# Kernel tuning notes

Hardware: AMD Instinct MI355X
Metric: run time of the kernel (lower is better)

The kernel has to match this reference:

```python
import jax, jax.numpy as jnp
import numpy as np

ALPHA = 0.2  # LeakyReLU negative slope
NEG_INF = jnp.float32(-9e15)


def gat_layer(h, mask, W, a, concat):
    """Dense GAT layer (pyGAT style). h: [B,N,Fin], mask: [N,N] bool, W: [Fin,Fout], a: [2*Fout,1]."""
    Wh = h @ W                                   # [B,N,Fout]
    F_out = W.shape[-1]
    e_src = Wh @ a[:F_out]                       # [B,N,1]
    e_dst = Wh @ a[F_out:]                       # [B,N,1]
    e = jax.nn.leaky_relu(e_src + jnp.swapaxes(e_dst, -1, -2), ALPHA)  # [B,N,N]
    att = jnp.where(mask, e, NEG_INF)
    att = jax.nn.softmax(att, axis=-1)
    out = att @ Wh                               # [B,N,Fout]
    return jax.nn.elu(out) if concat else out


def setup_inputs() -> dict:
    key = jax.random.key(0)
    ks = jax.random.split(key, 8)
    B, N, nfeat, nhid, nheads, emb, nclass = 4, 2048, 128, 64, 8, 64, 16
    slices = jax.random.normal(ks[0], (B, N, nfeat), jnp.float32)
    adj = jax.random.randint(ks[1], (N, N), 0, 2, jnp.int32)
    s = 1.0 / float(np.sqrt(nfeat))
    Ws = jax.random.uniform(ks[2], (nheads, nfeat, nhid), jnp.float32, -s, s)
    As = jax.random.uniform(ks[3], (nheads, 2 * nhid, 1), jnp.float32, -s, s)
    W1 = jax.random.uniform(ks[4], (nhid * nheads, emb), jnp.float32, -s, s)
    a1 = jax.random.uniform(ks[5], (2 * emb, 1), jnp.float32, -s, s)
    W2 = jax.random.uniform(ks[6], (emb, nclass), jnp.float32, -s, s)
    a2 = jax.random.uniform(ks[7], (2 * nclass, 1), jnp.float32, -s, s)
    return {"slices": slices, "adj": adj, "Ws": Ws, "As": As,
            "W1": W1, "a1": a1, "W2": W2, "a2": a2}


def reference(slices, adj, Ws, As, W1, a1, W2, a2):
    # Eval mode: dropout = 0 (identity).
    mask = adj > 0                               # [N,N], broadcasts over batch
    # Multi-head GAT with concat=True (ELU inside each head), vectorized over heads.
    heads = jax.vmap(lambda W, a: gat_layer(slices, mask, W, a, True))(Ws, As)  # [H,B,N,nhid]
    H, B, N, nh = heads.shape
    x = jnp.moveaxis(heads, 0, 2).reshape(B, N, H * nh)  # concat along features, head-major
    image_feature = jax.nn.elu(gat_layer(x, mask, W1, a1, False))              # [B,N,emb]
    pre = jax.nn.elu(gat_layer(image_feature, mask, W2, a2, False))            # [B,N,nclass]
    pre = pre[:, 0, :]                                                         # [B,nclass]
    return image_feature, pre
```

## Files before the change

### kernel.cpp

```cpp
#include <hip/hip_runtime.h>
#include <hip/hip_bf16.h>
#include <cstdint>


#define NN 2048

typedef float f32x4 __attribute__((ext_vector_type(4)));
typedef __bf16 bf16x8 __attribute__((ext_vector_type(8)));
typedef _Float16 f16;
typedef _Float16 f16x8 __attribute__((ext_vector_type(8)));

__device__ __forceinline__ unsigned pkbf(float a, float b) {
  __hip_bfloat162 t = __float22bfloat162_rn(make_float2(a, b));
  unsigned r;
  __builtin_memcpy(&r, &t, 4);
  return r;
}

__global__ __launch_bounds__(256) void prep_k(
    const int* __restrict__ adj, unsigned short* __restrict__ plane,
    const float* __restrict__ Ws, __bf16* __restrict__ WsFh, __bf16* __restrict__ WsFl,
    const float* __restrict__ W1, __bf16* __restrict__ W1Fh, __bf16* __restrict__ W1Fl) {
  const int bx = blockIdx.x, t = threadIdx.x;
  if (bx < 2048) {
    const long base = (long)bx * NN;
#pragma unroll
    for (int jt = 0; jt < 8; ++jt) {
      const int j = jt * 256 + t;
      plane[base + j] = adj[base + j] > 0 ? 0xFFFFu : 0u;
    }
  } else if (bx < 2304) {
    const int idx = (bx - 2048) * 256 + t;
    const int inst = idx >> 13;
    const int rem = idx & 8191;
    const int k = rem >> 6, n = rem & 63;
    const float v = Ws[(long)inst * 8192 + rem];
    const __bf16 vh = (__bf16)v;
    const int pos = ((k >> 5) * 4 + (n >> 4)) * 512 + (((k >> 3) & 3) * 16 + (n & 15)) * 8 + (k & 7);
    WsFh[(long)inst * 8192 + pos] = vh;
    WsFl[(long)inst * 8192 + pos] = (__bf16)(v - (float)vh);
  } else {
    const int idx = (bx - 2304) * 256 + t;
    const int k = idx >> 6, n = idx & 63;
    const float v = W1[idx];
    const __bf16 vh = (__bf16)v;
    const int pos = ((k >> 5) * 4 + (n >> 4)) * 512 + (((k >> 3) & 3) * 16 + (n & 15)) * 8 + (k & 7);
    W1Fh[pos] = vh;
    W1Fl[pos] = (__bf16)(v - (float)vh);
  }
}

struct GemmLd {
  float4 a0, a1;
  bf16x8 bh[4], bl[4];
};

__global__ __launch_bounds__(128) void gemm_mfma_k(
    const float* __restrict__ Aall, const __bf16* __restrict__ WFhi,
    const __bf16* __restrict__ WFlo, const float* __restrict__ avecAll,
    f16* __restrict__ WhBAll, float* __restrict__ Eo, float* __restrict__ Go,
    f16* __restrict__ Fo, f16* __restrict__ Ho, float* __restrict__ pC,
    int K, int KS, long aStrideB) {
  const int p = blockIdx.y;
  const int ks = blockIdx.z;
  const float* A = Aall + (long)(p & 3) * aStrideB;
  const long wfOff = (long)(p >> 2) * K * 64;
  const bf16x8* BhF = (const bf16x8*)(WFhi + wfOff);
  const bf16x8* BlF = (const bf16x8*)(WFlo + wfOff);

  const int t = threadIdx.x, lane = t & 63, wave = t >> 6;
  const int quad = lane >> 4, lm = lane & 15;
  const int i0w = blockIdx.x * 32 + wave * 16;
  const float* Arow = A + (long)(i0w + lm) * K;
  const int kBeg = ks * (K / KS), kEnd = kBeg + K / KS;

  f32x4 acc[4];
#pragma unroll
  for (int nt = 0; nt < 4; ++nt) acc[nt] = (f32x4){0.f, 0.f, 0.f, 0.f};

  auto LOAD = [&](GemmLd& L, int k0) {
    L.a0 = *(const float4*)(Arow + k0 + quad * 8);
    L.a1 = *(const float4*)(Arow + k0 + quad * 8 + 4);
    const int bbase = (k0 >> 5) * 256 + lane;
#pragma unroll
    for (int nt = 0; nt < 4; ++nt) {
      L.bh[nt] = BhF[bbase + nt * 64];
      L.bl[nt] = BlF[bbase + nt * 64];
    }
  };
  auto STEP = [&](const GemmLd& L) {
    const float av8[8] = {L.a0.x, L.a0.y, L.a0.z, L.a0.w, L.a1.x, L.a1.y, L.a1.z, L.a1.w};
    bf16x8 ah, al;
#pragma unroll
    for (int j = 0; j < 8; ++j) {
      const __bf16 h = (__bf16)av8[j];
      ah[j] = h;
      al[j] = (__bf16)(av8[j] - (float)h);
    }
#pragma unroll
    for (int nt = 0; nt < 4; ++nt) {
      acc[nt] = __builtin_amdgcn_mfma_f32_16x16x32_bf16(ah, L.bh[nt], acc[nt], 0, 0, 0);
      acc[nt] = __builtin_amdgcn_mfma_f32_16x16x32_bf16(al, L.bh[nt], acc[nt], 0, 0, 0);
      acc[nt] = __builtin_amdgcn_mfma_f32_16x16x32_bf16(ah, L.bl[nt], acc[nt], 0, 0, 0);
    }
  };

  GemmLd La, Lb;
  LOAD(La, kBeg);
  for (int k0 = kBeg; k0 < kEnd; k0 += 64) {
    LOAD(Lb, k0 + 32);
    STEP(La);
    LOAD(La, (k0 + 64 < kEnd) ? k0 + 64 : kBeg);
    STEP(Lb);
  }

  if (KS > 1) {
    float* pc = pC + ((long)(p * KS + ks) * NN) * 64;
#pragma unroll
    for (int reg = 0; reg < 4; ++reg) {
      const int row = i0w + quad * 4 + reg;
#pragma unroll
      for (int nt = 0; nt < 4; ++nt) pc[(long)row * 64 + nt * 16 + lm] = acc[nt][reg];
    }
    return;
  }

  const float* av = avecAll + (long)(p >> 2) * 128;
  f16* WhB = WhBAll + (long)p * NN * 64;
  float* E = Eo + (long)p * NN;
  float* G = Go + (long)p * NN;
  f16* F = Fo + (long)p * NN;
  f16* Hh = Ho + (long)p * NN;

  float alo[4], ahi[4];
#pragma unroll
  for (int nt = 0; nt < 4; ++nt) {
    alo[nt] = av[nt * 16 + lm];
    ahi[nt] = av[64 + nt * 16 + lm];
  }
#pragma unroll
  for (int reg = 0; reg < 4; ++reg) {
    float es = 0.f, ed = 0.f;
#pragma unroll
    for (int nt = 0; nt < 4; ++nt) {
      es += acc[nt][reg] * alo[nt];
      ed += acc[nt][reg] * ahi[nt];
    }
#pragma unroll
    for (int m = 1; m < 16; m <<= 1) {
      es += __shfl_xor(es, m);
      ed += __shfl_xor(ed, m);
    }
    if (lm == 0) {
      const int r = i0w + quad * 4 + reg;
      E[r] = __expf(es);
      G[r] = __expf(0.2f * es);
      F[r] = (f16)__expf(ed);
      Hh[r] = (f16)__expf(0.2f * ed);
    }
  }

  const int r0 = i0w + quad * 4;
  const long base = ((long)(r0 >> 5) * 4) * 512 + (((r0 >> 3) & 3) * 16 + lm) * 8 + (r0 & 7);
#pragma unroll
  for (int nt = 0; nt < 4; ++nt) {
    union { f16 h[4]; uint2 u; } pk;
#pragma unroll
    for (int q = 0; q < 4; ++q) pk.h[q] = (f16)acc[nt][q];
    *(uint2*)(WhB + base + nt * 512) = pk.u;
  }
}

__global__ __launch_bounds__(256) void gemm_epi_k(
    const float* __restrict__ pC, const float* __restrict__ avec,
    f16* __restrict__ WhBAll, float* __restrict__ Eo, float* __restrict__ Go,
    f16* __restrict__ Fo, f16* __restrict__ Ho, int KS) {
  const int inst = blockIdx.y;
  const int t = threadIdx.x;
  const int row = blockIdx.x * 16 + (t >> 4);
  const int cg = t & 15;
  f32x4 c = (f32x4){0.f, 0.f, 0.f, 0.f};
  for (int ks = 0; ks < KS; ++ks)
    c += *(const f32x4*)(pC + (((long)(inst * KS + ks) * NN) + row) * 64 + cg * 4);
  float es = 0.f, ed = 0.f;
#pragma unroll
  for (int q = 0; q < 4; ++q) {
    const int n = cg * 4 + q;
    es += c[q] * avec[n];
    ed += c[q] * avec[64 + n];
  }
#pragma unroll
  for (int m = 1; m < 16; m <<= 1) {
    es += __shfl_xor(es, m);
    ed += __shfl_xor(ed, m);
  }
  if (cg == 0) {
    Eo[(long)inst * NN + row] = __expf(es);
    Go[(long)inst * NN + row] = __expf(0.2f * es);
    Fo[(long)inst * NN + row] = (f16)__expf(ed);
    Ho[(long)inst * NN + row] = (f16)__expf(0.2f * ed);
  }
  f16* WhB = WhBAll + (long)inst * NN * 64;
#pragma unroll
  for (int q = 0; q < 4; ++q) {
    const int n = cg * 4 + q;
    const int pos = ((row >> 5) * 4 + (n >> 4)) * 512 + (((row >> 3) & 3) * 16 + (n & 15)) * 8 + (row & 7);
    WhB[pos] = (f16)c[q];
  }
}

struct AttnLd {
  f16x8 F, H;
  uint4 m0, m1;
  f16x8 b[4];
};

__global__ __launch_bounds__(512) void attn_k(
    const f16* __restrict__ WhBAll, const float* __restrict__ Eb,
    const float* __restrict__ Gb, const f16* __restrict__ Fb,
    const f16* __restrict__ Hb, const unsigned short* __restrict__ plane,
    float* __restrict__ out1, float* __restrict__ out2, int rowStride, long strideB,
    int jsCount, float* __restrict__ partAcc, float* __restrict__ partSum) {
  const int p = blockIdx.z;
  const int js = blockIdx.y;
  const f16x8* bp = (const f16x8*)(WhBAll + (long)p * NN * 64);
  const float* E = Eb + (long)p * NN;
  const float* G = Gb + (long)p * NN;
  const f16* F = Fb + (long)p * NN;
  const f16* Hv = Hb + (long)p * NN;
  const int t = threadIdx.x, lane = t & 63, wave = t >> 6;
  const int rw = wave & 3;
  const int half = wave >> 2;
  const int quad = lane >> 4, lm = lane & 15;
  const int i0 = blockIdx.x * 128 + rw * 32;
  const int span = 64 / jsCount;
  const int kbBeg = js * span + half * (span / 2);
  const int kbEnd = kbBeg + span / 2;

  const f16 e0 = (f16)E[i0 + lm], g0 = (f16)G[i0 + lm];
  const f16 e1 = (f16)E[i0 + 16 + lm], g1 = (f16)G[i0 + 16 + lm];
  f16x8 e0v, g0v, e1v, g1v;
#pragma unroll
  for (int j = 0; j < 8; ++j) { e0v[j] = e0; g0v[j] = g0; e1v[j] = e1; g1v[j] = g1; }
  const unsigned short* mp0 = plane + (long)(i0 + lm) * NN;
  const unsigned short* mp1 = plane + (long)(i0 + 16 + lm) * NN;

  f16x8 ones;
#pragma unroll
  for (int j = 0; j < 8; ++j) ones[j] = (lm == 0) ? (f16)1.0f : (f16)0.0f;

  f32x4 acc0[4], acc1[4], sum0, sum1;
#pragma unroll
  for (int nt = 0; nt < 4; ++nt) {
    acc0[nt] = (f32x4){0.f, 0.f, 0.f, 0.f};
    acc1[nt] = (f32x4){0.f, 0.f, 0.f, 0.f};
  }
  sum0 = (f32x4){0.f, 0.f, 0.f, 0.f};
  sum1 = (f32x4){0.f, 0.f, 0.f, 0.f};

  auto LOAD = [&](AttnLd& L, int kb) {
    const int c0 = kb * 32 + quad * 8;
    L.F = *(const f16x8*)(F + c0);
    L.H = *(const f16x8*)(Hv + c0);
    L.m0 = *(const uint4*)(mp0 + c0);
    L.m1 = *(const uint4*)(mp1 + c0);
#pragma unroll
    for (int nt = 0; nt < 4; ++nt) L.b[nt] = bp[(kb * 4 + nt) * 64 + lane];
  };
  auto STEP = [&](const AttnLd& L) {
    union { f16x8 v; uint4 u; } A0, A1;
    A0.v = __builtin_elementwise_max(e0v * L.F, g0v * L.H);
    A1.v = __builtin_elementwise_max(e1v * L.F, g1v * L.H);
    A0.u.x &= L.m0.x; A0.u.y &= L.m0.y; A0.u.z &= L.m0.z; A0.u.w &= L.m0.w;
    A1.u.x &= L.m1.x; A1.u.y &= L.m1.y; A1.u.z &= L.m1.z; A1.u.w &= L.m1.w;
#pragma unroll
    for (int nt = 0; nt < 4; ++nt) {
      acc0[nt] = __builtin_amdgcn_mfma_f32_16x16x32_f16(A0.v, L.b[nt], acc0[nt], 0, 0, 0);
      acc1[nt] = __builtin_amdgcn_mfma_f32_16x16x32_f16(A1.v, L.b[nt], acc1[nt], 0, 0, 0);
    }
    sum0 = __builtin_amdgcn_mfma_f32_16x16x32_f16(A0.v, ones, sum0, 0, 0, 0);
    sum1 = __builtin_amdgcn_mfma_f32_16x16x32_f16(A1.v, ones, sum1, 0, 0, 0);
  };

  AttnLd La, Lb;
  LOAD(La, kbBeg);
  for (int kb = kbBeg; kb < kbEnd; kb += 2) {
    LOAD(Lb, kb + 1);
    STEP(La);
    LOAD(La, (kb + 2 < kbEnd) ? kb + 2 : kbBeg);
    STEP(Lb);
  }

  __shared__ float cmb[4 * 64 * 40];
  if (half == 1) {
    float* dst = &cmb[(rw * 64 + lane) * 40];
#pragma unroll
    for (int nt = 0; nt < 4; ++nt) {
      *(f32x4*)(dst + nt * 4) = acc0[nt];
      *(f32x4*)(dst + 16 + nt * 4) = acc1[nt];
    }
    *(f32x4*)(dst + 32) = sum0;
    *(f32x4*)(dst + 36) = sum1;
  }
  __syncthreads();
  if (half == 1) return;
  {
    const float* src = &cmb[(rw * 64 + lane) * 40];
#pragma unroll
    for (int nt = 0; nt < 4; ++nt) {
      acc0[nt] += *(const f32x4*)(src + nt * 4);
      acc1[nt] += *(const f32x4*)(src + 16 + nt * 4);
    }
    sum0 += *(const f32x4*)(src + 32);
    sum1 += *(const f32x4*)(src + 36);
  }

  if (jsCount == 1) {
#pragma unroll
    for (int g = 0; g < 2; ++g) {
      const f32x4* acc = g ? acc1 : acc0;
      const f32x4 sm = g ? sum1 : sum0;
#pragma unroll
      for (int reg = 0; reg < 4; ++reg) {
        const int row = i0 + g * 16 + quad * 4 + reg;
        const float ls = __shfl(sm[reg], quad * 16);
        const float il = ls > 0.f ? 1.f / ls : 0.f;
#pragma unroll
        for (int nt = 0; nt < 4; ++nt) {
          float v = acc[nt][reg] * il;
          v = v > 0.f ? v : expm1f(v);
          const long o = (long)(p & 3) * strideB + (long)row * rowStride + (p >> 2) * 64 + nt * 16 + lm;
          out1[o] = v;
          if (out2) out2[o] = v;
        }
      }
    }
  } else {
    float* pAcc = partAcc + ((long)p * jsCount + js) * NN * 64;
    float* pSum = partSum + ((long)p * jsCount + js) * NN;
#pragma unroll
    for (int g = 0; g < 2; ++g) {
      const f32x4* acc = g ? acc1 : acc0;
      const f32x4 sm = g ? sum1 : sum0;
#pragma unroll
      for (int reg = 0; reg < 4; ++reg) {
        const int row = i0 + g * 16 + quad * 4 + reg;
#pragma unroll
        for (int nt = 0; nt < 4; ++nt) pAcc[(long)row * 64 + nt * 16 + lm] = acc[nt][reg];
        if (lm == 0) pSum[row] = sm[reg];
      }
    }
  }
}

__global__ __launch_bounds__(256) void combine_k(const float* __restrict__ partAcc,
                                                 const float* __restrict__ partSum,
                                                 float* __restrict__ img,
                                                 float* __restrict__ out, int JS) {
  const long idx = (long)blockIdx.x * 256 + threadIdx.x;
  const int cg = idx & 15;
  const int row = (int)((idx >> 4) & (NN - 1));
  const int inst = (int)(idx >> 15);
  f32x4 v = (f32x4){0.f, 0.f, 0.f, 0.f};
  float s = 0.f;
  for (int js = 0; js < JS; ++js) {
    const long b = ((long)inst * JS + js) * NN;
    v += *(const f32x4*)(partAcc + (b + row) * 64 + cg * 4);
    s += partSum[b + row];
  }
  const float il = s > 0.f ? 1.f / s : 0.f;
  f32x4 r;
#pragma unroll
  for (int q = 0; q < 4; ++q) {
    float x = v[q] * il;
    r[q] = x > 0.f ? x : expm1f(x);
  }
  const long o = ((long)inst * NN + row) * 64 + cg * 4;
  *(f32x4*)(img + o) = r;
  *(f32x4*)(out + o) = r;
}

__global__ __launch_bounds__(256) void layer3a_k(
    const float* __restrict__ img, const float* __restrict__ W2,
    const float* __restrict__ a2, const unsigned short* __restrict__ plane,
    float* __restrict__ pOut ) {
  const int bb = blockIdx.x, chunk = blockIdx.y, t = threadIdx.x;
  const float* A = img + (long)bb * NN * 64;
  __shared__ float w2alo[64], w2ahi[64];
  __shared__ float W2s[64][17];
  __shared__ float redc[4][17];
  if (t < 64) {
    float sl = 0.f, sh = 0.f;
#pragma unroll
    for (int c = 0; c < 16; ++c) {
      const float wv = W2[t * 16 + c];
      W2s[t][c] = wv;
      sl += wv * a2[c];
      sh += wv * a2[16 + c];
    }
    w2alo[t] = sl;
    w2ahi[t] = sh;
  }
  __syncthreads();

  float es = 0.f;
#pragma unroll 16
  for (int k = 0; k < 64; ++k) es += A[k] * w2alo[k];

  const int j = chunk * 256 + t;
  float arow[64];
#pragma unroll
  for (int q = 0; q < 16; ++q) *(f32x4*)(arow + q * 4) = *(const f32x4*)(A + (long)j * 64 + q * 4);
  float ed = 0.f;
#pragma unroll
  for (int k = 0; k < 64; ++k) ed += arow[k] * w2ahi[k];
  float e = es + ed;
  e = fmaxf(e, 0.2f * e);
  const float pv = plane[j] ? __expf(e) : 0.f;

  float acc[16];
#pragma unroll
  for (int c = 0; c < 16; ++c) {
    float wh = 0.f;
#pragma unroll
    for (int k = 0; k < 64; ++k) wh += arow[k] * W2s[k][c];
    acc[c] = pv * wh;
  }
  float lsum = pv;

#pragma unroll
  for (int off = 32; off > 0; off >>= 1) {
    lsum += __shfl_down(lsum, off);
#pragma unroll
    for (int c = 0; c < 16; ++c) acc[c] += __shfl_down(acc[c], off);
  }
  if ((t & 63) == 0) {
    const int wv = t >> 6;
#pragma unroll
    for (int c = 0; c < 16; ++c) redc[wv][c] = acc[c];
    redc[wv][16] = lsum;
  }
  __syncthreads();
  if (t < 17) {
    pOut[((long)bb * 8 + chunk) * 17 + t] =
        redc[0][t] + redc[1][t] + redc[2][t] + redc[3][t];
  }
}

__global__ __launch_bounds__(64) void layer3b_k(const float* __restrict__ pOut,
                                                float* __restrict__ outPre) {
  const int t = threadIdx.x;
  if (t >= 64) return;
  const int bb = t >> 4, c = t & 15;
  float a = 0.f, l = 0.f;
#pragma unroll
  for (int ch = 0; ch < 8; ++ch) {
    a += pOut[((long)bb * 8 + ch) * 17 + c];
    l += pOut[((long)bb * 8 + ch) * 17 + 16];
  }
  float v = a / l;
  v = v > 0.f ? v : expm1f(v);
  outPre[bb * 16 + c] = v;
}

extern "C" void kernel_launch(void* const* d_in, const int* in_sizes, int n_in,
                              void* d_out, int out_size, void* d_ws, size_t ws_size,
                              hipStream_t stream) {
  (void)in_sizes; (void)n_in; (void)out_size; (void)ws_size;
  constexpr int B = 4, N = NN, JS2 = 4, KS2 = 4;

  const float* slices = (const float*)d_in[0];
  const int* adj = (const int*)d_in[1];
  const float* Ws = (const float*)d_in[2];
  const float* As = (const float*)d_in[3];
  const float* W1 = (const float*)d_in[4];
  const float* a1 = (const float*)d_in[5];
  const float* W2 = (const float*)d_in[6];
  const float* a2 = (const float*)d_in[7];
  float* out = (float*)d_out;

  char* w = (char*)d_ws;
  size_t off = 0;
  auto alloc = [&](size_t bytes) {
    void* ptr = w + off;
    off += (bytes + 255) & ~(size_t)255;
    return ptr;
  };
  unsigned short* plane = (unsigned short*)alloc((size_t)N * N * 2);
  __bf16* WsFh = (__bf16*)alloc((size_t)8 * 128 * 64 * 2);
  __bf16* WsFl = (__bf16*)alloc((size_t)8 * 128 * 64 * 2);
  __bf16* W1Fh = (__bf16*)alloc((size_t)512 * 64 * 2);
  __bf16* W1Fl = (__bf16*)alloc((size_t)512 * 64 * 2);
  f16* WhB1 = (f16*)alloc((size_t)32 * N * 64 * 2);
  float* E1 = (float*)alloc((size_t)32 * N * 4);
  float* G1 = (float*)alloc((size_t)32 * N * 4);
  f16* F1 = (f16*)alloc((size_t)32 * N * 2);
  f16* H1 = (f16*)alloc((size_t)32 * N * 2);
  float* x = (float*)alloc((size_t)B * N * 512 * 4);
  float* pC2 = (float*)alloc((size_t)B * KS2 * N * 64 * 4);
  f16* WhB2 = (f16*)alloc((size_t)B * N * 64 * 2);
  float* E2 = (float*)alloc((size_t)B * N * 4);
  float* G2 = (float*)alloc((size_t)B * N * 4);
  f16* F2 = (f16*)alloc((size_t)B * N * 2);
  f16* H2 = (f16*)alloc((size_t)B * N * 2);
  float* img = (float*)alloc((size_t)B * N * 64 * 4);
  float* pAcc2 = (float*)alloc((size_t)B * JS2 * N * 64 * 4);
  float* pSum2 = (float*)alloc((size_t)B * JS2 * N * 4);
  float* pL3 = (float*)alloc((size_t)B * 8 * 17 * 4);

  prep_k<<<dim3(2432), dim3(256), 0, stream>>>(adj, plane, Ws, WsFh, WsFl, W1, W1Fh, W1Fl);

  gemm_mfma_k<<<dim3(N / 32, 32, 1), dim3(128), 0, stream>>>(
      slices, WsFh, WsFl, As, WhB1, E1, G1, F1, H1, (float*)nullptr,
      128, 1, (long)N * 128);
  attn_k<<<dim3(N / 128, 1, 32), dim3(512), 0, stream>>>(
      WhB1, E1, G1, F1, H1, plane, x, (float*)nullptr, 512, (long)N * 512,
      1, (float*)nullptr, (float*)nullptr);

  gemm_mfma_k<<<dim3(N / 32, 4, KS2), dim3(128), 0, stream>>>(
      x, W1Fh, W1Fl, a1, (f16*)nullptr, (float*)nullptr, (float*)nullptr,
      (f16*)nullptr, (f16*)nullptr, pC2, 512, KS2, (long)N * 512);
  gemm_epi_k<<<dim3(N / 16, 4), dim3(256), 0, stream>>>(
      pC2, a1, WhB2, E2, G2, F2, H2, KS2);
  attn_k<<<dim3(N / 128, JS2, 4), dim3(512), 0, stream>>>(
      WhB2, E2, G2, F2, H2, plane, (float*)nullptr, (float*)nullptr, 64, (long)N * 64,
      JS2, pAcc2, pSum2);
  combine_k<<<dim3(B * N * 16 / 256), dim3(256), 0, stream>>>(pAcc2, pSum2, img, out, JS2);

  layer3a_k<<<dim3(B, 8), dim3(256), 0, stream>>>(img, W2, a2, plane, pL3);
  layer3b_k<<<dim3(1), dim3(64), 0, stream>>>(pL3, out + (size_t)B * N * 64);
}
```

Baseline: 192.0 us.

## Stage attention operands in LDS via global_load_lds with byte-packed tiled mask

New measurement: 165.0 us. 14.0% less time.

```diff
diff --git a/kernel.cpp b/kernel.cpp
--- a/kernel.cpp
+++ b/kernel.cpp
@@ -10,24 +10,24 @@
 typedef _Float16 f16;
 typedef _Float16 f16x8 __attribute__((ext_vector_type(8)));
 
-__device__ __forceinline__ unsigned pkbf(float a, float b) {
-  __hip_bfloat162 t = __float22bfloat162_rn(make_float2(a, b));
-  unsigned r;
-  __builtin_memcpy(&r, &t, 4);
-  return r;
+__device__ __forceinline__ void gll16(const void* g, void* l) {
+  __builtin_amdgcn_global_load_lds(
+      (const __attribute__((address_space(1))) unsigned int*)g,
+      (__attribute__((address_space(3))) unsigned int*)l, 16, 0, 0);
 }
 
 __global__ __launch_bounds__(256) void prep_k(
-    const int* __restrict__ adj, unsigned short* __restrict__ plane,
+    const int* __restrict__ adj, unsigned char* __restrict__ pm,
     const float* __restrict__ Ws, __bf16* __restrict__ WsFh, __bf16* __restrict__ WsFl,
     const float* __restrict__ W1, __bf16* __restrict__ W1Fh, __bf16* __restrict__ W1Fl) {
   const int bx = blockIdx.x, t = threadIdx.x;
   if (bx < 2048) {
-    const long base = (long)bx * NN;
+    const int i = bx;
 #pragma unroll
     for (int jt = 0; jt < 8; ++jt) {
       const int j = jt * 256 + t;
-      plane[base + j] = adj[base + j] > 0 ? 0xFFFFu : 0u;
+      pm[((long)(j >> 5) << 16) + i * 32 + (j & 31)] =
+          adj[(long)i * NN + j] > 0 ? 0xFFu : 0u;
     }
   } else if (bx < 2304) {
     const int idx = (bx - 2048) * 256 + t;
@@ -209,45 +209,59 @@
   }
 }
 
-struct AttnLd {
-  f16x8 F, H;
-  uint4 m0, m1;
-  f16x8 b[4];
-};
-
 __global__ __launch_bounds__(512) void attn_k(
     const f16* __restrict__ WhBAll, const float* __restrict__ Eb,
     const float* __restrict__ Gb, const f16* __restrict__ Fb,
-    const f16* __restrict__ Hb, const unsigned short* __restrict__ plane,
+    const f16* __restrict__ Hb, const unsigned char* __restrict__ pm,
     float* __restrict__ out1, float* __restrict__ out2, int rowStride, long strideB,
     int jsCount, float* __restrict__ partAcc, float* __restrict__ partSum) {
   const int p = blockIdx.z;
   const int js = blockIdx.y;
-  const f16x8* bp = (const f16x8*)(WhBAll + (long)p * NN * 64);
+  const f16* WhB = WhBAll + (long)p * NN * 64;
   const float* E = Eb + (long)p * NN;
   const float* G = Gb + (long)p * NN;
   const f16* F = Fb + (long)p * NN;
   const f16* Hv = Hb + (long)p * NN;
   const int t = threadIdx.x, lane = t & 63, wave = t >> 6;
-  const int rw = wave & 3;
-  const int half = wave >> 2;
+  const int rw = wave & 3, half = wave >> 2;
   const int quad = lane >> 4, lm = lane & 15;
-  const int i0 = blockIdx.x * 128 + rw * 32;
+  const int i0 = blockIdx.x * 128;
+  const int rbase = rw * 32;
   const int span = 64 / jsCount;
-  const int kbBeg = js * span + half * (span / 2);
-  const int kbEnd = kbBeg + span / 2;
-
-  const f16 e0 = (f16)E[i0 + lm], g0 = (f16)G[i0 + lm];
-  const f16 e1 = (f16)E[i0 + 16 + lm], g1 = (f16)G[i0 + 16 + lm];
+  const int nIter = span / 2;
+  const int kbBeg = js * span + half * nIter;
+
+  __shared__ __align__(16) char pool[40960];
+  f16* Fs = (f16*)pool;
+  f16* Hs = (f16*)(pool + 4096);
+  char* ring = pool + 8192 + half * 16384;
+
+  const int r0g = i0 + rbase + lm, r1g = i0 + rbase + 16 + lm;
+  const f16 e0 = (f16)E[r0g], g0 = (f16)G[r0g];
+  const f16 e1 = (f16)E[r1g], g1 = (f16)G[r1g];
   f16x8 e0v, g0v, e1v, g1v;
 #pragma unroll
   for (int j = 0; j < 8; ++j) { e0v[j] = e0; g0v[j] = g0; e1v[j] = e1; g1v[j] = g1; }
-  const unsigned short* mp0 = plane + (long)(i0 + lm) * NN;
-  const unsigned short* mp1 = plane + (long)(i0 + 16 + lm) * NN;
 
   f16x8 ones;
 #pragma unroll
   for (int j = 0; j < 8; ++j) ones[j] = (lm == 0) ? (f16)1.0f : (f16)0.0f;
+
+  if (wave == 0) {
+#pragma unroll
+    for (int q = 0; q < 4; ++q) gll16((const char*)F + q * 1024 + lane * 16, pool + q * 1024);
+#pragma unroll
+    for (int q = 0; q < 4; ++q) gll16((const char*)Hv + q * 1024 + lane * 16, pool + 4096 + q * 1024);
+  }
+  if (rw == 0) {
+    const char* gB = (const char*)WhB + (long)kbBeg * 4096;
+    const unsigned char* gM = pm + ((long)kbBeg << 16) + i0 * 32;
+#pragma unroll
+    for (int q = 0; q < 4; ++q) gll16(gB + q * 1024 + lane * 16, ring + q * 1024);
+#pragma unroll
+    for (int q = 0; q < 4; ++q) gll16(gM + q * 1024 + lane * 16, ring + 4096 + q * 1024);
+  }
+  __syncthreads();
 
   f32x4 acc0[4], acc1[4], sum0, sum1;
 #pragma unroll
@@ -258,40 +272,47 @@
   sum0 = (f32x4){0.f, 0.f, 0.f, 0.f};
   sum1 = (f32x4){0.f, 0.f, 0.f, 0.f};
 
-  auto LOAD = [&](AttnLd& L, int kb) {
-    const int c0 = kb * 32 + quad * 8;
-    L.F = *(const f16x8*)(F + c0);
-    L.H = *(const f16x8*)(Hv + c0);
-    L.m0 = *(const uint4*)(mp0 + c0);
-    L.m1 = *(const uint4*)(mp1 + c0);
-#pragma unroll
-    for (int nt = 0; nt < 4; ++nt) L.b[nt] = bp[(kb * 4 + nt) * 64 + lane];
-  };
-  auto STEP = [&](const AttnLd& L) {
+  for (int i = 0; i < nIter; ++i) {
+    const int kb = kbBeg + i;
+    if (rw == 0 && i + 1 < nIter) {
+      char* dst = ring + ((i + 1) & 1) * 8192;
+      const char* gB = (const char*)WhB + (long)(kb + 1) * 4096;
+      const unsigned char* gM = pm + ((long)(kb + 1) << 16) + i0 * 32;
+#pragma unroll
+      for (int q = 0; q < 4; ++q) gll16(gB + q * 1024 + lane * 16, dst + q * 1024);
+#pragma unroll
+      for (int q = 0; q < 4; ++q) gll16(gM + q * 1024 + lane * 16, dst + 4096 + q * 1024);
+    }
+    const char* slot = ring + (i & 1) * 8192;
+    const f16x8 F8 = *(const f16x8*)(Fs + kb * 32 + quad * 8);
+    const f16x8 H8 = *(const f16x8*)(Hs + kb * 32 + quad * 8);
+    const uint2 m0 = *(const uint2*)(slot + 4096 + (rbase + lm) * 32 + quad * 8);
+    const uint2 m1 = *(const uint2*)(slot + 4096 + (rbase + 16 + lm) * 32 + quad * 8);
+
     union { f16x8 v; uint4 u; } A0, A1;
-    A0.v = __builtin_elementwise_max(e0v * L.F, g0v * L.H);
-    A1.v = __builtin_elementwise_max(e1v * L.F, g1v * L.H);
-    A0.u.x &= L.m0.x; A0.u.y &= L.m0.y; A0.u.z &= L.m0.z; A0.u.w &= L.m0.w;
-    A1.u.x &= L.m1.x; A1.u.y &= L.m1.y; A1.u.z &= L.m1.z; A1.u.w &= L.m1.w;
+    A0.v = __builtin_elementwise_max(e0v * F8, g0v * H8);
+    A1.v = __builtin_elementwise_max(e1v * F8, g1v * H8);
+    A0.u.x &= __builtin_amdgcn_perm(0u, m0.x, 0x01010000u);
+    A0.u.y &= __builtin_amdgcn_perm(0u, m0.x, 0x03030202u);
+    A0.u.z &= __builtin_amdgcn_perm(0u, m0.y, 0x01010000u);
+    A0.u.w &= __builtin_amdgcn_perm(0u, m0.y, 0x03030202u);
+    A1.u.x &= __builtin_amdgcn_perm(0u, m1.x, 0x01010000u);
+    A1.u.y &= __builtin_amdgcn_perm(0u, m1.x, 0x03030202u);
+    A1.u.z &= __builtin_amdgcn_perm(0u, m1.y, 0x01010000u);
+    A1.u.w &= __builtin_amdgcn_perm(0u, m1.y, 0x03030202u);
+
 #pragma unroll
     for (int nt = 0; nt < 4; ++nt) {
-      acc0[nt] = __builtin_amdgcn_mfma_f32_16x16x32_f16(A0.v, L.b[nt], acc0[nt], 0, 0, 0);
-      acc1[nt] = __builtin_amdgcn_mfma_f32_16x16x32_f16(A1.v, L.b[nt], acc1[nt], 0, 0, 0);
+      const f16x8 bfr = *(const f16x8*)(slot + (nt * 64 + lane) * 16);
+      acc0[nt] = __builtin_amdgcn_mfma_f32_16x16x32_f16(A0.v, bfr, acc0[nt], 0, 0, 0);
+      acc1[nt] = __builtin_amdgcn_mfma_f32_16x16x32_f16(A1.v, bfr, acc1[nt], 0, 0, 0);
     }
     sum0 = __builtin_amdgcn_mfma_f32_16x16x32_f16(A0.v, ones, sum0, 0, 0, 0);
     sum1 = __builtin_amdgcn_mfma_f32_16x16x32_f16(A1.v, ones, sum1, 0, 0, 0);
-  };
-
-  AttnLd La, Lb;
-  LOAD(La, kbBeg);
-  for (int kb = kbBeg; kb < kbEnd; kb += 2) {
-    LOAD(Lb, kb + 1);
-    STEP(La);
-    LOAD(La, (kb + 2 < kbEnd) ? kb + 2 : kbBeg);
-    STEP(Lb);
-  }
-
-  __shared__ float cmb[4 * 64 * 40];
+    __syncthreads();
+  }
+
+  float* cmb = (float*)pool;
   if (half == 1) {
     float* dst = &cmb[(rw * 64 + lane) * 40];
 #pragma unroll
@@ -322,7 +343,7 @@
       const f32x4 sm = g ? sum1 : sum0;
 #pragma unroll
       for (int reg = 0; reg < 4; ++reg) {
-        const int row = i0 + g * 16 + quad * 4 + reg;
+        const int row = i0 + rbase + g * 16 + quad * 4 + reg;
         const float ls = __shfl(sm[reg], quad * 16);
         const float il = ls > 0.f ? 1.f / ls : 0.f;
 #pragma unroll
@@ -344,7 +365,7 @@
       const f32x4 sm = g ? sum1 : sum0;
 #pragma unroll
       for (int reg = 0; reg < 4; ++reg) {
-        const int row = i0 + g * 16 + quad * 4 + reg;
+        const int row = i0 + rbase + g * 16 + quad * 4 + reg;
 #pragma unroll
         for (int nt = 0; nt < 4; ++nt) pAcc[(long)row * 64 + nt * 16 + lm] = acc[nt][reg];
         if (lm == 0) pSum[row] = sm[reg];
@@ -382,7 +403,7 @@
 
 __global__ __launch_bounds__(256) void layer3a_k(
     const float* __restrict__ img, const float* __restrict__ W2,
-    const float* __restrict__ a2, const unsigned short* __restrict__ plane,
+    const float* __restrict__ a2, const unsigned char* __restrict__ pm,
     float* __restrict__ pOut ) {
   const int bb = blockIdx.x, chunk = blockIdx.y, t = threadIdx.x;
   const float* A = img + (long)bb * NN * 64;
@@ -416,7 +437,7 @@
   for (int k = 0; k < 64; ++k) ed += arow[k] * w2ahi[k];
   float e = es + ed;
   e = fmaxf(e, 0.2f * e);
-  const float pv = plane[j] ? __expf(e) : 0.f;
+  const float pv = pm[((long)(j >> 5) << 16) + (j & 31)] ? __expf(e) : 0.f;
 
   float acc[16];
 #pragma unroll
@@ -486,7 +507,7 @@
     off += (bytes + 255) & ~(size_t)255;
     return ptr;
   };
-  unsigned short* plane = (unsigned short*)alloc((size_t)N * N * 2);
+  unsigned char* pm = (unsigned char*)alloc((size_t)64 * 65536);
   __bf16* WsFh = (__bf16*)alloc((size_t)8 * 128 * 64 * 2);
   __bf16* WsFl = (__bf16*)alloc((size_t)8 * 128 * 64 * 2);
   __bf16* W1Fh = (__bf16*)alloc((size_t)512 * 64 * 2);
@@ -508,13 +529,13 @@
   float* pSum2 = (float*)alloc((size_t)B * JS2 * N * 4);
   float* pL3 = (float*)alloc((size_t)B * 8 * 17 * 4);
 
-  prep_k<<<dim3(2432), dim3(256), 0, stream>>>(adj, plane, Ws, WsFh, WsFl, W1, W1Fh, W1Fl);
+  prep_k<<<dim3(2432), dim3(256), 0, stream>>>(adj, pm, Ws, WsFh, WsFl, W1, W1Fh, W1Fl);
 
   gemm_mfma_k<<<dim3(N / 32, 32, 1), dim3(128), 0, stream>>>(
       slices, WsFh, WsFl, As, WhB1, E1, G1, F1, H1, (float*)nullptr,
       128, 1, (long)N * 128);
   attn_k<<<dim3(N / 128, 1, 32), dim3(512), 0, stream>>>(
-      WhB1, E1, G1, F1, H1, plane, x, (float*)nullptr, 512, (long)N * 512,
+      WhB1, E1, G1, F1, H1, pm, x, (float*)nullptr, 512, (long)N * 512,
       1, (float*)nullptr, (float*)nullptr);
 
   gemm_mfma_k<<<dim3(N / 32, 4, KS2), dim3(128), 0, stream>>>(
@@ -523,10 +544,10 @@
   gemm_epi_k<<<dim3(N / 16, 4), dim3(256), 0, stream>>>(
       pC2, a1, WhB2, E2, G2, F2, H2, KS2);
   attn_k<<<dim3(N / 128, JS2, 4), dim3(512), 0, stream>>>(
-      WhB2, E2, G2, F2, H2, plane, (float*)nullptr, (float*)nullptr, 64, (long)N * 64,
+      WhB2, E2, G2, F2, H2, pm, (float*)nullptr, (float*)nullptr, 64, (long)N * 64,
       JS2, pAcc2, pSum2);
   combine_k<<<dim3(B * N * 16 / 256), dim3(256), 0, stream>>>(pAcc2, pSum2, img, out, JS2);
 
-  layer3a_k<<<dim3(B, 8), dim3(256), 0, stream>>>(img, W2, a2, plane, pL3);
+  layer3a_k<<<dim3(B, 8), dim3(256), 0, stream>>>(img, W2, a2, pm, pL3);
   layer3b_k<<<dim3(1), dim3(64), 0, stream>>>(pL3, out + (size_t)B * N * 64);
 }
```
